# Performance work log

Hardware: AMD Instinct MI355X
Metric: run time of the kernel (lower is better)

## Reference

```python
import jax, jax.numpy as jnp
import numpy as np
from math import sqrt

N_HEADS = 16

def _rope(t, freqs):
    # t: [b, n, l, hd]; freqs: [l, hd//2, 2] (real, imag of unit rotations)
    b, n, l, hd = t.shape
    t2 = t.reshape(b, n, l, hd // 2, 2)
    tr, ti = t2[..., 0], t2[..., 1]
    fr, fi = freqs[..., 0], freqs[..., 1]  # broadcast over b, n
    out_r = tr * fr - ti * fi
    out_i = tr * fi + ti * fr
    return jnp.stack([out_r, out_i], axis=-1).reshape(b, n, l, hd)

def setup_inputs() -> dict:
    key = jax.random.key(0)
    ks = jax.random.split(key, 6)
    B, L, D = 2, 2048, 1024
    HD = D // N_HEADS
    x = jax.random.normal(ks[0], (B, L, D), dtype=jnp.float32)
    # proper rotary frequencies: theta_i = 10000^{-2i/hd}, angle = pos * theta
    inv = 1.0 / (10000.0 ** (np.arange(0, HD, 2, dtype=np.float32) / HD))  # [HD//2]
    ang = np.arange(L, dtype=np.float32)[:, None] * inv[None, :]           # [L, HD//2]
    freqs = jnp.asarray(np.stack([np.cos(ang), np.sin(ang)], axis=-1))     # [L, HD//2, 2]
    # additive causal mask
    causal = jnp.tril(jnp.ones((L, L), dtype=bool))
    attention_mask = jnp.where(causal, 0.0, -1e9).astype(jnp.float32)[None, None]
    init = 1.0 / sqrt(D)
    Wq = jax.random.normal(ks[1], (D, D), dtype=jnp.float32) * init
    Wk = jax.random.normal(ks[2], (D, D), dtype=jnp.float32) * init
    Wv = jax.random.normal(ks[3], (D, D), dtype=jnp.float32) * init
    Wo = jax.random.normal(ks[4], (D, D), dtype=jnp.float32) * init
    return {"x": x, "freqs": freqs, "attention_mask": attention_mask,
            "Wq": Wq, "Wk": Wk, "Wv": Wv, "Wo": Wo}

def reference(x, freqs, attention_mask, Wq, Wk, Wv, Wo):
    b, l, d = x.shape
    n = N_HEADS
    hd = d // n
    scale = sqrt(hd)

    def split_heads(t):  # [b, l, d] -> [b, n, l, hd]
        return t.reshape(b, l, n, hd).transpose(0, 2, 1, 3)

    q = split_heads(x @ Wq.T)
    k = split_heads(x @ Wk.T)
    v = split_heads(x @ Wv.T)
    q = _rope(q, freqs)
    k = _rope(k, freqs)
    scores = jnp.einsum('bnqd,bnkd->bnqk', q, k) / scale
    attn = jax.nn.softmax(scores + attention_mask, axis=-1)
    out = jnp.einsum('bnqk,bnkd->bnqd', attn, v)
    out = out.transpose(0, 2, 1, 3).reshape(b, l, d)
    return out @ Wo.T
```

## Files before the change

### kernel.cpp

```cpp
#include <hip/hip_runtime.h>
#include <stdint.h>

#define LSEQ 2048
#define DMODEL 1024
#define NHEADS 16
#define HDIM 64
#define MROWS 4096

typedef __attribute__((ext_vector_type(8))) short short8;
typedef __attribute__((ext_vector_type(4))) float f32x4;

static __device__ __forceinline__ unsigned short f2bf(float f) {
    unsigned u = __builtin_bit_cast(unsigned, f);
    u += 0x7fffu + ((u >> 16) & 1u);
    return (unsigned short)(u >> 16);
}

static __device__ __forceinline__ void gl2lds16(const unsigned short* g, unsigned short* l) {
    __builtin_amdgcn_global_load_lds(
        (const __attribute__((address_space(1))) unsigned int*)g,
        (__attribute__((address_space(3))) unsigned int*)l, 16, 0, 0);
}

__global__ void cast_all(const float* __restrict__ x,  const float* __restrict__ Wq,
                         const float* __restrict__ Wk, const float* __restrict__ Wv,
                         const float* __restrict__ Wo,
                         unsigned short* __restrict__ xb,
                         unsigned short* __restrict__ wqkv,
                         unsigned short* __restrict__ wo) {
    int i = blockIdx.x * blockDim.x + threadIdx.x;
    const float4* src;
    ushort4* dst;
    if (i < 1048576) {
        src = (const float4*)x + i;
        dst = (ushort4*)xb + i;
    } else {
        int t = i - 1048576;
        int w = t >> 18;
        int j = t & 262143;
        const float* s = (w == 0) ? Wq : (w == 1) ? Wk : (w == 2) ? Wv : Wo;
        src = (const float4*)s + j;
        dst = (w == 3) ? ((ushort4*)wo + j) : ((ushort4*)wqkv + (size_t)w * 262144 + j);
    }
    float4 v = *src;
    ushort4 o;
    o.x = f2bf(v.x); o.y = f2bf(v.y); o.z = f2bf(v.z); o.w = f2bf(v.w);
    *dst = o;
}

template <int TM, bool OUT_BF16>
__global__ __launch_bounds__(256) void gemm_nt(const unsigned short* __restrict__ A,
                                               const unsigned short* __restrict__ Bw,
                                               void* __restrict__ C,
                                               int Kdim, int ldc) {
    constexpr int WM = TM / 2;
    __shared__ unsigned short As[TM * 32];
    __shared__ unsigned short Bs[128 * 32];
    int tid = threadIdx.x;
    int lane = tid & 63, wave = tid >> 6;
    int row16 = lane & 15, quad = lane >> 4;
    int wm = wave & 1, wn = wave >> 1;
    int m0 = blockIdx.x * TM;
    int n0 = blockIdx.y * 128;

    int srow = wave * 16 + (lane >> 2);
    int scol = (lane & 3) * 8;
    const unsigned short* Ag = A  + (size_t)(m0 + srow) * Kdim + scol;
    const unsigned short* Bg = Bw + (size_t)(n0 + srow) * Kdim + scol;
    unsigned short* Asw = As + wave * 512;
    unsigned short* Bsw = Bs + wave * 512;

    f32x4 acc[WM / 16][4];
    #pragma unroll
    for (int i = 0; i < WM / 16; ++i)
        #pragma unroll
        for (int j = 0; j < 4; ++j) acc[i][j] = (f32x4){0.f, 0.f, 0.f, 0.f};

    for (int k0 = 0; k0 < Kdim; k0 += 32) {
        #pragma unroll
        for (int i = 0; i < TM / 64; ++i)
            gl2lds16(Ag + (size_t)i * 64 * Kdim + k0, Asw + i * 2048);
        gl2lds16(Bg + k0, Bsw);
        gl2lds16(Bg + (size_t)64 * Kdim + k0, Bsw + 2048);
        __syncthreads();

        short8 af[WM / 16], bf_[4];
        #pragma unroll
        for (int mi = 0; mi < WM / 16; ++mi)
            af[mi] = *(const short8*)(As + (wm * WM + mi * 16 + row16) * 32 + quad * 8);
        #pragma unroll
        for (int ni = 0; ni < 4; ++ni)
            bf_[ni] = *(const short8*)(Bs + (wn * 64 + ni * 16 + row16) * 32 + quad * 8);
        #pragma unroll
        for (int mi = 0; mi < WM / 16; ++mi)
            #pragma unroll
            for (int ni = 0; ni < 4; ++ni)
                acc[mi][ni] = __builtin_amdgcn_mfma_f32_16x16x32_bf16(af[mi], bf_[ni], acc[mi][ni], 0, 0, 0);
        __syncthreads();
    }

    int orow = m0 + wm * WM + quad * 4;
    int ocol = n0 + wn * 64 + row16;
    #pragma unroll
    for (int mi = 0; mi < WM / 16; ++mi)
        #pragma unroll
        for (int ni = 0; ni < 4; ++ni)
            #pragma unroll
            for (int r = 0; r < 4; ++r) {
                size_t idx = (size_t)(orow + mi * 16 + r) * ldc + (ocol + ni * 16);
                if (OUT_BF16) ((unsigned short*)C)[idx] = f2bf(acc[mi][ni][r]);
                else          ((float*)C)[idx]          = acc[mi][ni][r];
            }
}

__global__ __launch_bounds__(256) void gemm_qkv(const unsigned short* __restrict__ A,
                                                const unsigned short* __restrict__ Bw,
                                                const float* __restrict__ freqs,
                                                unsigned short* __restrict__ qh,
                                                unsigned short* __restrict__ kh,
                                                unsigned short* __restrict__ vt) {
    const int Kdim = DMODEL;
    __shared__ unsigned short As[128 * 32];
    __shared__ unsigned short Bs[128 * 32];
    int tid = threadIdx.x;
    int lane = tid & 63, wave = tid >> 6;
    int row16 = lane & 15, quad = lane >> 4;
    int wm = wave & 1, wn = wave >> 1;
    int m0 = blockIdx.x * 128;
    int n0 = blockIdx.y * 128;

    int srow = wave * 16 + (lane >> 2);
    int scol = (lane & 3) * 8;
    const unsigned short* Ag  = A  + (size_t)(m0 + srow) * Kdim + scol;
    const unsigned short* Ag2 = Ag + (size_t)64 * Kdim;
    const unsigned short* Bg  = Bw + (size_t)(n0 + srow) * Kdim + scol;
    const unsigned short* Bg2 = Bg + (size_t)64 * Kdim;
    unsigned short* Asw = As + wave * 512;
    unsigned short* Bsw = Bs + wave * 512;

    f32x4 acc[4][4];
    #pragma unroll
    for (int i = 0; i < 4; ++i)
        #pragma unroll
        for (int j = 0; j < 4; ++j) acc[i][j] = (f32x4){0.f, 0.f, 0.f, 0.f};

    for (int k0 = 0; k0 < Kdim; k0 += 32) {
        gl2lds16(Ag  + k0, Asw);
        gl2lds16(Ag2 + k0, Asw + 2048);
        gl2lds16(Bg  + k0, Bsw);
        gl2lds16(Bg2 + k0, Bsw + 2048);
        __syncthreads();

        short8 af[4], bf_[4];
        #pragma unroll
        for (int mi = 0; mi < 4; ++mi)
            af[mi] = *(const short8*)(As + (wm * 64 + mi * 16 + row16) * 32 + quad * 8);
        #pragma unroll
        for (int ni = 0; ni < 4; ++ni)
            bf_[ni] = *(const short8*)(Bs + (wn * 64 + ni * 16 + row16) * 32 + quad * 8);
        #pragma unroll
        for (int mi = 0; mi < 4; ++mi)
            #pragma unroll
            for (int ni = 0; ni < 4; ++ni)
                acc[mi][ni] = __builtin_amdgcn_mfma_f32_16x16x32_bf16(af[mi], bf_[ni], acc[mi][ni], 0, 0, 0);
        __syncthreads();
    }

    int orow = m0 + wm * 64 + quad * 4;
    int ocol = n0 + wn * 64 + row16;
    int b = m0 >> 11;
    int region = n0 >> 10;

    if (region < 2) {
        unsigned short* dst = region ? kh : qh;
        int cbase = ocol - region * 1024;
        float sgn = (row16 & 1) ? 1.f : -1.f;
        #pragma unroll
        for (int ni = 0; ni < 4; ++ni) {
            int c = cbase + ni * 16;
            int head = c >> 6, d = c & 63, ii = d >> 1;
            unsigned short* hb = dst + (((size_t)(b * NHEADS + head)) * LSEQ) * HDIM + d;
            #pragma unroll
            for (int mi = 0; mi < 4; ++mi)
                #pragma unroll
                for (int r = 0; r < 4; ++r) {
                    int l = (orow + mi * 16 + r) & 2047;
                    float own = acc[mi][ni][r];
                    float par = __shfl_xor(own, 1);
                    float2 f = *(const float2*)(freqs + ((size_t)l * 32 + ii) * 2);
                    float out = own * f.x + par * (sgn * f.y);
                    hb[(size_t)l * HDIM] = f2bf(out);
                }
        }
    } else {
        #pragma unroll
        for (int ni = 0; ni < 4; ++ni) {
            int c = ocol - 2048 + ni * 16;
            int head = c >> 6, d = c & 63;
            size_t vbase = (((size_t)(b * NHEADS + head)) * HDIM + d) * LSEQ;
            #pragma unroll
            for (int mi = 0; mi < 4; ++mi) {
                int l0 = (orow + mi * 16) & 2047;
                ushort4 o;
                o.x = f2bf(acc[mi][ni][0]);
                o.y = f2bf(acc[mi][ni][1]);
                o.z = f2bf(acc[mi][ni][2]);
                o.w = f2bf(acc[mi][ni][3]);
                *(ushort4*)(vt + vbase + l0) = o;
            }
        }
    }
}

__global__ __launch_bounds__(256) void attn_flash(const unsigned short* __restrict__ qh,
                                                  const unsigned short* __restrict__ kh,
                                                  const unsigned short* __restrict__ vt,
                                                  unsigned short* __restrict__ oh) {
    __shared__ unsigned short Ks[2][64 * 32];
    __shared__ unsigned short Vs[2][64 * 32];
    __shared__ unsigned short Ps[4][1024];
    const float CS = 0.18033688011112042f;
    const float CB = 28.853900817779268f;
    int lane  = threadIdx.x & 63;
    int wave  = threadIdx.x >> 6;
    int row16 = lane & 15, quad = lane >> 4;
    int id  = blockIdx.x;
    int xcd = id & 7;
    int bn  = xcd * 4 + ((id >> 3) & 3);
    int pairidx = id >> 5;
    int b = bn >> 4, n = bn & 15;

    const unsigned short* Qb = qh + (size_t)bn * LSEQ * HDIM;
    const unsigned short* Kb = kh + (size_t)bn * LSEQ * HDIM;
    const unsigned short* Vb = vt + (size_t)bn * HDIM * LSEQ;
    unsigned short* pw = Ps[wave];

    int srow = wave * 16 + row16;
    int scol = quad * 8;

    #pragma unroll
    for (int half = 0; half < 2; ++half) {
        int qb = half ? (31 - pairidx) : pairidx;
        int q0 = qb * 64 + wave * 16;
        int qabs = q0 + row16;
        const unsigned short* Qr = Qb + (size_t)(q0 + row16) * HDIM + quad * 8;
        short8 bq0 = *(const short8*)(Qr);
        short8 bq1 = *(const short8*)(Qr + 32);

        f32x4 accO[4];
        #pragma unroll
        for (int i = 0; i < 4; ++i) accO[i] = (f32x4){0.f, 0.f, 0.f, 0.f};
        float l_s = 0.f;

        int nk = qb + 1;
        for (int kt = 0; kt < nk; ++kt) {
            int k0 = kt * 64;
            #pragma unroll
            for (int h = 0; h < 2; ++h) {
                gl2lds16(Kb + (size_t)(k0 + srow) * HDIM + h * 32 + scol, Ks[h] + wave * 512);
                gl2lds16(Vb + (size_t)srow * LSEQ + k0 + h * 32 + scol,   Vs[h] + wave * 512);
            }
            __syncthreads();

            f32x4 z[4];
            #pragma unroll
            for (int kg = 0; kg < 4; ++kg) {
                short8 af0 = *(const short8*)(Ks[0] + kg * 512 + lane * 8);
                short8 af1 = *(const short8*)(Ks[1] + kg * 512 + lane * 8);
                f32x4 zz = (f32x4){0.f, 0.f, 0.f, 0.f};
                zz = __builtin_amdgcn_mfma_f32_16x16x32_bf16(af0, bq0, zz, 0, 0, 0);
                zz = __builtin_amdgcn_mfma_f32_16x16x32_bf16(af1, bq1, zz, 0, 0, 0);
                z[kg] = zz;
            }

            float p[4][4];
            if (kt == nk - 1) {
                #pragma unroll
                for (int kg = 0; kg < 4; ++kg)
                    #pragma unroll
                    for (int rr = 0; rr < 4; ++rr) {
                        float e = __builtin_amdgcn_exp2f(z[kg][rr] * CS - CB);
                        bool msk = (k0 + kg * 16 + quad * 4 + rr > qabs);
                        p[kg][rr] = msk ? 0.f : e;
                    }
            } else {
                #pragma unroll
                for (int kg = 0; kg < 4; ++kg)
                    #pragma unroll
                    for (int rr = 0; rr < 4; ++rr)
                        p[kg][rr] = __builtin_amdgcn_exp2f(z[kg][rr] * CS - CB);
            }
            #pragma unroll
            for (int kg = 0; kg < 4; ++kg)
                l_s += (p[kg][0] + p[kg][1]) + (p[kg][2] + p[kg][3]);

            #pragma unroll
            for (int kg = 0; kg < 4; ++kg) {
                uint2 w;
                w.x = (unsigned)f2bf(p[kg][0]) | ((unsigned)f2bf(p[kg][1]) << 16);
                w.y = (unsigned)f2bf(p[kg][2]) | ((unsigned)f2bf(p[kg][3]) << 16);
                *(uint2*)(pw + kg * 256 + (quad >> 1) * 128 + row16 * 8 + (quad & 1) * 4) = w;
            }
            asm volatile("s_waitcnt lgkmcnt(0)" ::: "memory");
            short8 bp0 = *(const short8*)(pw + lane * 8);
            short8 bp1 = *(const short8*)(pw + 512 + lane * 8);

            #pragma unroll
            for (int dg = 0; dg < 4; ++dg) {
                short8 vf0 = *(const short8*)(Vs[0] + dg * 512 + lane * 8);
                short8 vf1 = *(const short8*)(Vs[1] + dg * 512 + lane * 8);
                accO[dg] = __builtin_amdgcn_mfma_f32_16x16x32_bf16(vf0, bp0, accO[dg], 0, 0, 0);
                accO[dg] = __builtin_amdgcn_mfma_f32_16x16x32_bf16(vf1, bp1, accO[dg], 0, 0, 0);
            }
            __syncthreads();
        }

        float ls = l_s;
        ls += __shfl_xor(ls, 16);
        ls += __shfl_xor(ls, 32);
        float inv = 1.0f / ls;
        #pragma unroll
        for (int di = 0; di < 4; ++di) {
            ushort4 o;
            o.x = f2bf(accO[di][0] * inv);
            o.y = f2bf(accO[di][1] * inv);
            o.z = f2bf(accO[di][2] * inv);
            o.w = f2bf(accO[di][3] * inv);
            *(ushort4*)(oh + (size_t)(b * LSEQ + q0 + row16) * DMODEL + n * HDIM + di * 16 + quad * 4) = o;
        }
    }
}

extern "C" void kernel_launch(void* const* d_in, const int* in_sizes, int n_in,
                              void* d_out, int out_size, void* d_ws, size_t ws_size,
                              hipStream_t stream) {
    const float* x     = (const float*)d_in[0];
    const float* freqs = (const float*)d_in[1];
    const float* Wq = (const float*)d_in[3];
    const float* Wk = (const float*)d_in[4];
    const float* Wv = (const float*)d_in[5];
    const float* Wo = (const float*)d_in[6];

    char* ws = (char*)d_ws;
    unsigned short* xb   = (unsigned short*)ws; ws += (size_t)MROWS * DMODEL * 2;
    unsigned short* wqkv = (unsigned short*)ws; ws += (size_t)3 * DMODEL * DMODEL * 2;
    unsigned short* wo   = (unsigned short*)ws; ws += (size_t)DMODEL * DMODEL * 2;
    unsigned short* qh   = (unsigned short*)ws; ws += (size_t)32 * LSEQ * HDIM * 2;
    unsigned short* kh   = (unsigned short*)ws; ws += (size_t)32 * LSEQ * HDIM * 2;
    unsigned short* vt   = (unsigned short*)ws; ws += (size_t)32 * HDIM * LSEQ * 2;
    unsigned short* oh   = (unsigned short*)ws; ws += (size_t)MROWS * DMODEL * 2;

    cast_all<<<8192, 256, 0, stream>>>(x, Wq, Wk, Wv, Wo, xb, wqkv, wo);

    gemm_qkv<<<dim3(MROWS / 128, 3072 / 128), 256, 0, stream>>>(xb, wqkv, freqs, qh, kh, vt);

    attn_flash<<<512, 256, 0, stream>>>(qh, kh, vt, oh);

    gemm_nt<64, false><<<dim3(MROWS / 64, DMODEL / 128), 256, 0, stream>>>(oh, wo, (float*)d_out, DMODEL, DMODEL);
}
```

Before: 214.1 us.

## Double-buffer K/V tiles and process two adjacent query blocks per workgroup

The attention kernel now has each workgroup handle two adjacent 64-row query blocks (a 128-row span) instead of a mirrored pair. Each staged K/V tile is reused by both query blocks, and K/V loads are double-buffered so the next tile's global-to-LDS copy overlaps the current compute. Workgroups are balanced by pairing small and large spans through the qb mapping. This costs twice the LDS for K/V and more registers for the second accumulator set and the cached fragments, which may lower occupancy.

```diff
diff --git a/kernel.cpp b/kernel.cpp
--- a/kernel.cpp
+++ b/kernel.cpp
@@ -216,18 +216,20 @@
                                                   const unsigned short* __restrict__ kh,
                                                   const unsigned short* __restrict__ vt,
                                                   unsigned short* __restrict__ oh) {
-    __shared__ unsigned short Ks[2][64 * 32];
-    __shared__ unsigned short Vs[2][64 * 32];
+    __shared__ unsigned short Ks[2][2][2048];
+    __shared__ unsigned short Vs[2][2][2048];
     __shared__ unsigned short Ps[4][1024];
     const float CS = 0.18033688011112042f;
     const float CB = 28.853900817779268f;
     int lane  = threadIdx.x & 63;
     int wave  = threadIdx.x >> 6;
     int row16 = lane & 15, quad = lane >> 4;
-    int id  = blockIdx.x;
-    int xcd = id & 7;
-    int bn  = xcd * 4 + ((id >> 3) & 3);
-    int pairidx = id >> 5;
+    int id   = blockIdx.x;
+    int xcd  = id & 7;
+    int pidx = id >> 3;
+    int bn   = xcd * 4 + (pidx & 3);
+    int t    = pidx >> 2;
+    int qb   = (t < 8) ? t : 23 - t;
     int b = bn >> 4, n = bn & 15;
 
     const unsigned short* Qb = qh + (size_t)bn * LSEQ * HDIM;
@@ -235,46 +237,65 @@
     const unsigned short* Vb = vt + (size_t)bn * HDIM * LSEQ;
     unsigned short* pw = Ps[wave];
 
+    int q0a = qb * 128 + wave * 16;
+    int q0b = q0a + 64;
+    const unsigned short* Qra = Qb + (size_t)(q0a + row16) * HDIM + quad * 8;
+    const unsigned short* Qrb = Qb + (size_t)(q0b + row16) * HDIM + quad * 8;
+    short8 bqa0 = *(const short8*)(Qra);
+    short8 bqa1 = *(const short8*)(Qra + 32);
+    short8 bqb0 = *(const short8*)(Qrb);
+    short8 bqb1 = *(const short8*)(Qrb + 32);
+
+    f32x4 accA[4], accB[4];
+    #pragma unroll
+    for (int i = 0; i < 4; ++i) {
+        accA[i] = (f32x4){0.f, 0.f, 0.f, 0.f};
+        accB[i] = (f32x4){0.f, 0.f, 0.f, 0.f};
+    }
+    float lsA = 0.f, lsB = 0.f;
+    int qabsA = q0a + row16, qabsB = q0b + row16;
+
     int srow = wave * 16 + row16;
     int scol = quad * 8;
-
-    #pragma unroll
-    for (int half = 0; half < 2; ++half) {
-        int qb = half ? (31 - pairidx) : pairidx;
-        int q0 = qb * 64 + wave * 16;
-        int qabs = q0 + row16;
-        const unsigned short* Qr = Qb + (size_t)(q0 + row16) * HDIM + quad * 8;
-        short8 bq0 = *(const short8*)(Qr);
-        short8 bq1 = *(const short8*)(Qr + 32);
-
-        f32x4 accO[4];
-        #pragma unroll
-        for (int i = 0; i < 4; ++i) accO[i] = (f32x4){0.f, 0.f, 0.f, 0.f};
-        float l_s = 0.f;
-
-        int nk = qb + 1;
-        for (int kt = 0; kt < nk; ++kt) {
-            int k0 = kt * 64;
+    int nk = 2 * qb + 2;
+
+    auto stage = [&](int kt, int buf) {
+        int k0 = kt * 64;
+        #pragma unroll
+        for (int h = 0; h < 2; ++h) {
+            gl2lds16(Kb + (size_t)(k0 + srow) * HDIM + h * 32 + scol, &Ks[buf][h][wave * 512]);
+            gl2lds16(Vb + (size_t)srow * LSEQ + k0 + h * 32 + scol,   &Vs[buf][h][wave * 512]);
+        }
+    };
+
+    stage(0, 0);
+    for (int kt = 0; kt < nk; ++kt) {
+        int buf = kt & 1;
+        int k0 = kt * 64;
+        __syncthreads();
+        if (kt + 1 < nk) stage(kt + 1, buf ^ 1);
+
+        short8 kf[4][2], vf[4][2];
+        #pragma unroll
+        for (int g = 0; g < 4; ++g)
             #pragma unroll
             for (int h = 0; h < 2; ++h) {
-                gl2lds16(Kb + (size_t)(k0 + srow) * HDIM + h * 32 + scol, Ks[h] + wave * 512);
-                gl2lds16(Vb + (size_t)srow * LSEQ + k0 + h * 32 + scol,   Vs[h] + wave * 512);
-            }
-            __syncthreads();
-
+                kf[g][h] = *(const short8*)(&Ks[buf][h][g * 512 + lane * 8]);
+                vf[g][h] = *(const short8*)(&Vs[buf][h][g * 512 + lane * 8]);
+            }
+
+        auto qstep = [&](short8 bq0, short8 bq1, f32x4* accO, float& l_s,
+                         int qabs, bool edge) {
             f32x4 z[4];
             #pragma unroll
             for (int kg = 0; kg < 4; ++kg) {
-                short8 af0 = *(const short8*)(Ks[0] + kg * 512 + lane * 8);
-                short8 af1 = *(const short8*)(Ks[1] + kg * 512 + lane * 8);
                 f32x4 zz = (f32x4){0.f, 0.f, 0.f, 0.f};
-                zz = __builtin_amdgcn_mfma_f32_16x16x32_bf16(af0, bq0, zz, 0, 0, 0);
-                zz = __builtin_amdgcn_mfma_f32_16x16x32_bf16(af1, bq1, zz, 0, 0, 0);
+                zz = __builtin_amdgcn_mfma_f32_16x16x32_bf16(kf[kg][0], bq0, zz, 0, 0, 0);
+                zz = __builtin_amdgcn_mfma_f32_16x16x32_bf16(kf[kg][1], bq1, zz, 0, 0, 0);
                 z[kg] = zz;
             }
-
             float p[4][4];
-            if (kt == nk - 1) {
+            if (edge) {
                 #pragma unroll
                 for (int kg = 0; kg < 4; ++kg)
                     #pragma unroll
@@ -304,18 +325,23 @@
             asm volatile("s_waitcnt lgkmcnt(0)" ::: "memory");
             short8 bp0 = *(const short8*)(pw + lane * 8);
             short8 bp1 = *(const short8*)(pw + 512 + lane * 8);
-
             #pragma unroll
             for (int dg = 0; dg < 4; ++dg) {
-                short8 vf0 = *(const short8*)(Vs[0] + dg * 512 + lane * 8);
-                short8 vf1 = *(const short8*)(Vs[1] + dg * 512 + lane * 8);
-                accO[dg] = __builtin_amdgcn_mfma_f32_16x16x32_bf16(vf0, bp0, accO[dg], 0, 0, 0);
-                accO[dg] = __builtin_amdgcn_mfma_f32_16x16x32_bf16(vf1, bp1, accO[dg], 0, 0, 0);
-            }
-            __syncthreads();
-        }
-
-        float ls = l_s;
+                accO[dg] = __builtin_amdgcn_mfma_f32_16x16x32_bf16(vf[dg][0], bp0, accO[dg], 0, 0, 0);
+                accO[dg] = __builtin_amdgcn_mfma_f32_16x16x32_bf16(vf[dg][1], bp1, accO[dg], 0, 0, 0);
+            }
+        };
+
+        qstep(bqb0, bqb1, accB, lsB, qabsB, kt == nk - 1);
+        if (kt <= 2 * qb)
+            qstep(bqa0, bqa1, accA, lsA, qabsA, kt == 2 * qb);
+    }
+
+    #pragma unroll
+    for (int half = 0; half < 2; ++half) {
+        f32x4* accO = half ? accB : accA;
+        float ls = half ? lsB : lsA;
+        int q0 = half ? q0b : q0a;
         ls += __shfl_xor(ls, 16);
         ls += __shfl_xor(ls, 32);
         float inv = 1.0f / ls;
```

Result: slower. 221.2 us (+3.3%).

## Rewrite flash attention with 32x32 MFMA, key-split waves and register P shuffle

Applied to the files above, without the earlier changes.

Restructures the attention kernel so each block handles one 64-row query tile with four waves split 2x2 over query halves and key halves. It switches to 32x32x16 MFMA and moves P between lanes with cross-lane shuffles instead of an LDS round trip. Partial outputs from the two key halves are merged through shared memory at the end. It also doubles the grid with a longest-first tile order, skips fully masked sub-tiles on the diagonal, and sets an occupancy hint. This aims to cut LDS traffic and improve load balance, at the cost of an extra reduction step and more accumulator registers.

```diff
diff --git a/kernel.cpp b/kernel.cpp
--- a/kernel.cpp
+++ b/kernel.cpp
@@ -9,11 +9,15 @@
 
 typedef __attribute__((ext_vector_type(8))) short short8;
 typedef __attribute__((ext_vector_type(4))) float f32x4;
+typedef __attribute__((ext_vector_type(16))) float f32x16;
 
 static __device__ __forceinline__ unsigned short f2bf(float f) {
     unsigned u = __builtin_bit_cast(unsigned, f);
     u += 0x7fffu + ((u >> 16) & 1u);
     return (unsigned short)(u >> 16);
+}
+static __device__ __forceinline__ unsigned packbf2(float a, float b) {
+    return (unsigned)f2bf(a) | ((unsigned)f2bf(b) << 16);
 }
 
 static __device__ __forceinline__ void gl2lds16(const unsigned short* g, unsigned short* l) {
@@ -212,122 +216,153 @@
     }
 }
 
-__global__ __launch_bounds__(256) void attn_flash(const unsigned short* __restrict__ qh,
-                                                  const unsigned short* __restrict__ kh,
-                                                  const unsigned short* __restrict__ vt,
-                                                  unsigned short* __restrict__ oh) {
-    __shared__ unsigned short Ks[2][64 * 32];
-    __shared__ unsigned short Vs[2][64 * 32];
-    __shared__ unsigned short Ps[4][1024];
+__global__ __launch_bounds__(256, 4) void attn_flash(const unsigned short* __restrict__ qh,
+                                                     const unsigned short* __restrict__ kh,
+                                                     const unsigned short* __restrict__ vt,
+                                                     unsigned short* __restrict__ oh) {
+    __shared__ char smem[16896];
+    unsigned short* Kbuf = (unsigned short*)smem;
+    unsigned short* Vbuf = (unsigned short*)(smem + 8192);
+    float* mO = (float*)smem;
+    float* mL = (float*)(smem + 16384);
     const float CS = 0.18033688011112042f;
     const float CB = 28.853900817779268f;
-    int lane  = threadIdx.x & 63;
-    int wave  = threadIdx.x >> 6;
-    int row16 = lane & 15, quad = lane >> 4;
+
+    int lane = threadIdx.x & 63;
+    int wave = threadIdx.x >> 6;
+    int l31 = lane & 31;
+    int h   = lane >> 5;
+    int kq  = wave >> 1, qq = wave & 1;
+
     int id  = blockIdx.x;
     int xcd = id & 7;
     int bn  = xcd * 4 + ((id >> 3) & 3);
-    int pairidx = id >> 5;
+    int s   = id >> 5;
+    int u = s & 7, rnd = s >> 3;
+    int qb = (rnd == 0) ? (31 - u) : (rnd == 1) ? (16 + u) : (rnd == 2) ? (15 - u) : u;
     int b = bn >> 4, n = bn & 15;
 
     const unsigned short* Qb = qh + (size_t)bn * LSEQ * HDIM;
     const unsigned short* Kb = kh + (size_t)bn * LSEQ * HDIM;
     const unsigned short* Vb = vt + (size_t)bn * HDIM * LSEQ;
-    unsigned short* pw = Ps[wave];
-
-    int srow = wave * 16 + row16;
-    int scol = quad * 8;
-
-    #pragma unroll
-    for (int half = 0; half < 2; ++half) {
-        int qb = half ? (31 - pairidx) : pairidx;
-        int q0 = qb * 64 + wave * 16;
-        int qabs = q0 + row16;
-        const unsigned short* Qr = Qb + (size_t)(q0 + row16) * HDIM + quad * 8;
-        short8 bq0 = *(const short8*)(Qr);
-        short8 bq1 = *(const short8*)(Qr + 32);
-
-        f32x4 accO[4];
-        #pragma unroll
-        for (int i = 0; i < 4; ++i) accO[i] = (f32x4){0.f, 0.f, 0.f, 0.f};
-        float l_s = 0.f;
-
-        int nk = qb + 1;
-        for (int kt = 0; kt < nk; ++kt) {
-            int k0 = kt * 64;
-            #pragma unroll
-            for (int h = 0; h < 2; ++h) {
-                gl2lds16(Kb + (size_t)(k0 + srow) * HDIM + h * 32 + scol, Ks[h] + wave * 512);
-                gl2lds16(Vb + (size_t)srow * LSEQ + k0 + h * 32 + scol,   Vs[h] + wave * 512);
-            }
-            __syncthreads();
-
-            f32x4 z[4];
-            #pragma unroll
-            for (int kg = 0; kg < 4; ++kg) {
-                short8 af0 = *(const short8*)(Ks[0] + kg * 512 + lane * 8);
-                short8 af1 = *(const short8*)(Ks[1] + kg * 512 + lane * 8);
-                f32x4 zz = (f32x4){0.f, 0.f, 0.f, 0.f};
-                zz = __builtin_amdgcn_mfma_f32_16x16x32_bf16(af0, bq0, zz, 0, 0, 0);
-                zz = __builtin_amdgcn_mfma_f32_16x16x32_bf16(af1, bq1, zz, 0, 0, 0);
-                z[kg] = zz;
-            }
-
-            float p[4][4];
-            if (kt == nk - 1) {
+
+    int q0 = qb * 64;
+    int qabs = q0 + qq * 32 + l31;
+
+    short8 qf[4];
+    #pragma unroll
+    for (int mf = 0; mf < 4; ++mf)
+        qf[mf] = *(const short8*)(Qb + (size_t)(q0 + qq * 32 + l31) * HDIM + mf * 16 + h * 8);
+
+    int sf  = wave >> 1;
+    int m0s = (wave & 1) * 2;
+    const unsigned short* kg = Kb + (size_t)(sf * 32 + l31) * HDIM + m0s * 16 + h * 8;
+    const unsigned short* vg = Vb + (size_t)(sf * 32 + l31) * LSEQ + m0s * 16 + h * 8;
+    unsigned short* kds = Kbuf + (sf * 4 + m0s) * 512;
+    unsigned short* vds = Vbuf + (sf * 4 + m0s) * 512;
+
+    f32x16 accO[2];
+    #pragma unroll
+    for (int i = 0; i < 16; ++i) { accO[0][i] = 0.f; accO[1][i] = 0.f; }
+    float l_s = 0.f;
+
+    int nk = qb + 1;
+    for (int kt = 0; kt < nk; ++kt) {
+        const unsigned short* kgk = kg + (size_t)kt * 64 * HDIM;
+        const unsigned short* vgk = vg + kt * 64;
+        gl2lds16(kgk, kds);       gl2lds16(kgk + 16, kds + 512);
+        gl2lds16(vgk, vds);       gl2lds16(vgk + 16, vds + 512);
+        __syncthreads();
+
+        bool edge = (kt == nk - 1);
+        bool dead = edge && (kq == 1) && (qq == 0);
+
+        if (!dead) {
+            f32x16 z;
+            #pragma unroll
+            for (int i = 0; i < 16; ++i) z[i] = 0.f;
+            #pragma unroll
+            for (int m = 0; m < 4; ++m) {
+                short8 kf = *(const short8*)(Kbuf + (kq * 4 + m) * 512 + lane * 8);
+                z = __builtin_amdgcn_mfma_f32_32x32x16_bf16(kf, qf[m], z, 0, 0, 0);
+            }
+
+            float p[16];
+            bool maskz = edge && (kq == qq);
+            #pragma unroll
+            for (int r = 0; r < 16; ++r) {
+                float e = __builtin_amdgcn_exp2f(z[r] * CS - CB);
+                if (maskz) {
+                    int kabs = kt * 64 + kq * 32 + (r & 3) + 8 * (r >> 2) + 4 * h;
+                    if (kabs > qabs) e = 0.f;
+                }
+                p[r] = e;
+            }
+            float ps = 0.f;
+            #pragma unroll
+            for (int r = 0; r < 16; ++r) ps += p[r];
+            l_s += ps;
+
+            uint2 P4[4];
+            #pragma unroll
+            for (int g = 0; g < 4; ++g) {
+                P4[g].x = packbf2(p[4 * g], p[4 * g + 1]);
+                P4[g].y = packbf2(p[4 * g + 2], p[4 * g + 3]);
+            }
+            short8 bfr[2];
+            bool hb = (h != 0);
+            #pragma unroll
+            for (int m = 0; m < 2; ++m) {
+                uint2 own = hb ? P4[1 + 2 * m] : P4[2 * m];
+                uint2 snd = hb ? P4[2 * m]     : P4[1 + 2 * m];
+                uint2 rcv;
+                rcv.x = __shfl_xor(snd.x, 32);
+                rcv.y = __shfl_xor(snd.y, 32);
+                uint4 bb;
+                bb.x = hb ? rcv.x : own.x;
+                bb.y = hb ? rcv.y : own.y;
+                bb.z = hb ? own.x : rcv.x;
+                bb.w = hb ? own.y : rcv.y;
+                bfr[m] = __builtin_bit_cast(short8, bb);
+            }
+
+            #pragma unroll
+            for (int dq = 0; dq < 2; ++dq)
                 #pragma unroll
-                for (int kg = 0; kg < 4; ++kg)
-                    #pragma unroll
-                    for (int rr = 0; rr < 4; ++rr) {
-                        float e = __builtin_amdgcn_exp2f(z[kg][rr] * CS - CB);
-                        bool msk = (k0 + kg * 16 + quad * 4 + rr > qabs);
-                        p[kg][rr] = msk ? 0.f : e;
-                    }
-            } else {
-                #pragma unroll
-                for (int kg = 0; kg < 4; ++kg)
-                    #pragma unroll
-                    for (int rr = 0; rr < 4; ++rr)
-                        p[kg][rr] = __builtin_amdgcn_exp2f(z[kg][rr] * CS - CB);
-            }
-            #pragma unroll
-            for (int kg = 0; kg < 4; ++kg)
-                l_s += (p[kg][0] + p[kg][1]) + (p[kg][2] + p[kg][3]);
-
-            #pragma unroll
-            for (int kg = 0; kg < 4; ++kg) {
-                uint2 w;
-                w.x = (unsigned)f2bf(p[kg][0]) | ((unsigned)f2bf(p[kg][1]) << 16);
-                w.y = (unsigned)f2bf(p[kg][2]) | ((unsigned)f2bf(p[kg][3]) << 16);
-                *(uint2*)(pw + kg * 256 + (quad >> 1) * 128 + row16 * 8 + (quad & 1) * 4) = w;
-            }
-            asm volatile("s_waitcnt lgkmcnt(0)" ::: "memory");
-            short8 bp0 = *(const short8*)(pw + lane * 8);
-            short8 bp1 = *(const short8*)(pw + 512 + lane * 8);
-
-            #pragma unroll
-            for (int dg = 0; dg < 4; ++dg) {
-                short8 vf0 = *(const short8*)(Vs[0] + dg * 512 + lane * 8);
-                short8 vf1 = *(const short8*)(Vs[1] + dg * 512 + lane * 8);
-                accO[dg] = __builtin_amdgcn_mfma_f32_16x16x32_bf16(vf0, bp0, accO[dg], 0, 0, 0);
-                accO[dg] = __builtin_amdgcn_mfma_f32_16x16x32_bf16(vf1, bp1, accO[dg], 0, 0, 0);
-            }
-            __syncthreads();
+                for (int m = 0; m < 2; ++m) {
+                    short8 vf = *(const short8*)(Vbuf + (dq * 4 + kq * 2 + m) * 512 + lane * 8);
+                    accO[dq] = __builtin_amdgcn_mfma_f32_32x32x16_bf16(vf, bfr[m], accO[dq], 0, 0, 0);
+                }
         }
-
-        float ls = l_s;
-        ls += __shfl_xor(ls, 16);
-        ls += __shfl_xor(ls, 32);
-        float inv = 1.0f / ls;
-        #pragma unroll
-        for (int di = 0; di < 4; ++di) {
-            ushort4 o;
-            o.x = f2bf(accO[di][0] * inv);
-            o.y = f2bf(accO[di][1] * inv);
-            o.z = f2bf(accO[di][2] * inv);
-            o.w = f2bf(accO[di][3] * inv);
-            *(ushort4*)(oh + (size_t)(b * LSEQ + q0 + row16) * DMODEL + n * HDIM + di * 16 + quad * 4) = o;
-        }
+        __syncthreads();
+    }
+
+    l_s += __shfl_xor(l_s, 32);
+
+    if (kq == 1) {
+        #pragma unroll
+        for (int dq = 0; dq < 2; ++dq)
+            #pragma unroll
+            for (int r = 0; r < 16; ++r)
+                mO[(qq * 2 + dq) * 1024 + r * 64 + lane] = accO[dq][r];
+        mL[qq * 64 + lane] = l_s;
+    }
+    __syncthreads();
+    if (kq == 0) {
+        float inv = 1.0f / (l_s + mL[qq * 64 + lane]);
+        #pragma unroll
+        for (int dq = 0; dq < 2; ++dq)
+            #pragma unroll
+            for (int g = 0; g < 4; ++g) {
+                float o0 = (accO[dq][4 * g]     + mO[(qq * 2 + dq) * 1024 + (4 * g)     * 64 + lane]) * inv;
+                float o1 = (accO[dq][4 * g + 1] + mO[(qq * 2 + dq) * 1024 + (4 * g + 1) * 64 + lane]) * inv;
+                float o2 = (accO[dq][4 * g + 2] + mO[(qq * 2 + dq) * 1024 + (4 * g + 2) * 64 + lane]) * inv;
+                float o3 = (accO[dq][4 * g + 3] + mO[(qq * 2 + dq) * 1024 + (4 * g + 3) * 64 + lane]) * inv;
+                ushort4 o;
+                o.x = f2bf(o0); o.y = f2bf(o1); o.z = f2bf(o2); o.w = f2bf(o3);
+                int d = dq * 32 + 8 * g + 4 * h;
+                *(ushort4*)(oh + (size_t)(b * LSEQ + q0 + qq * 32 + l31) * DMODEL + n * HDIM + d) = o;
+            }
     }
 }
 
@@ -354,7 +389,7 @@
 
     gemm_qkv<<<dim3(MROWS / 128, 3072 / 128), 256, 0, stream>>>(xb, wqkv, freqs, qh, kh, vt);
 
-    attn_flash<<<512, 256, 0, stream>>>(qh, kh, vt, oh);
+    attn_flash<<<1024, 256, 0, stream>>>(qh, kh, vt, oh);
 
     gemm_nt<64, false><<<dim3(MROWS / 64, DMODEL / 128), 256, 0, stream>>>(oh, wo, (float*)d_out, DMODEL, DMODEL);
 }
```

New measurement: 210.0 us. Within noise of the previous version (-1.9%).
